# Performance work log

Hardware: AMD Instinct MI355X
Metric: run time of the kernel (lower is better)

The kernel has to match this reference:

```python
import jax, jax.numpy as jnp
import numpy as np

INPUT_DIM = 1024
NUM_HEADS = 16
HEAD_DIM = INPUT_DIM // NUM_HEADS


def setup_inputs() -> dict:
    key = jax.random.key(0)
    ks = jax.random.split(key, 9)
    d = INPUT_DIM
    s = 1.0 / np.sqrt(d)
    x = jax.random.normal(ks[0], (2, 2048, d), dtype=jnp.float32)
    # nn.Linear default init ~ U(-1/sqrt(in), 1/sqrt(in)); weights stored as (out, in), we keep (in, out)
    Wq = jax.random.uniform(ks[1], (d, d), jnp.float32, -s, s)
    bq = jax.random.uniform(ks[2], (d,), jnp.float32, -s, s)
    Wk = jax.random.uniform(ks[3], (d, d), jnp.float32, -s, s)
    bk = jax.random.uniform(ks[4], (d,), jnp.float32, -s, s)
    Wv = jax.random.uniform(ks[5], (d, d), jnp.float32, -s, s)
    bv = jax.random.uniform(ks[6], (d,), jnp.float32, -s, s)
    Wo = jax.random.uniform(ks[7], (d, d), jnp.float32, -s, s)
    bo = jax.random.uniform(ks[8], (d,), jnp.float32, -s, s)
    return {"x": x, "Wq": Wq, "bq": bq, "Wk": Wk, "bk": bk, "Wv": Wv, "bv": bv, "Wo": Wo, "bo": bo}


def reference(x, Wq, bq, Wk, bk, Wv, bv, Wo, bo):
    b, t, d = x.shape
    h, hd = NUM_HEADS, HEAD_DIM
    # projections -> [b, h, t, hd]
    q = (x @ Wq + bq).reshape(b, t, h, hd).transpose(0, 2, 1, 3)
    k = (x @ Wk + bk).reshape(b, t, h, hd).transpose(0, 2, 1, 3)
    v = (x @ Wv + bv).reshape(b, t, h, hd).transpose(0, 2, 1, 3)
    scores = jnp.einsum('bhqd,bhkd->bhqk', q, k) / jnp.sqrt(jnp.float32(hd))
    probs = jax.nn.softmax(scores, axis=-1)
    out = jnp.einsum('bhqk,bhkd->bhqd', probs, v)
    out = out.transpose(0, 2, 1, 3).reshape(b, t, d)
    return out @ Wo + bo
```

## Files before the change

kernel.cpp:

```cpp
#include <hip/hip_runtime.h>
#include <math.h>


#define BATCH 2
#define SEQ   2048
#define DIM   1024
#define NHEAD 16
#define HDIM  64
#define MROWS (BATCH * SEQ)
#define BH    (BATCH * NHEAD)
#define NSPLIT 2
#define TILES_PER_SPLIT (SEQ / 64 / NSPLIT)

typedef __attribute__((ext_vector_type(4))) float     floatx4;
typedef __attribute__((ext_vector_type(4))) float     float4v;
typedef __attribute__((ext_vector_type(8))) _Float16  half8;
typedef __attribute__((ext_vector_type(4))) _Float16  half4;
typedef __attribute__((ext_vector_type(2))) __fp16    fp16x2;
typedef __attribute__((ext_vector_type(4))) unsigned  uint4v;

#define SOFT_C 5.77078016f
#define QSCALE 0.18033688f

#if __has_builtin(__builtin_amdgcn_exp2f)
#define EXP2F(x) __builtin_amdgcn_exp2f(x)
#else
#define EXP2F(x) exp2f(x)
#endif

__device__ __forceinline__ void gload16(const void* g, void* l) {
    __builtin_amdgcn_global_load_lds(
        (const __attribute__((address_space(1))) unsigned int*)g,
        (__attribute__((address_space(3))) unsigned int*)l, 16, 0, 0);
}

__device__ __forceinline__ unsigned pk2(float a, float b) {
    fp16x2 v = __builtin_amdgcn_cvt_pkrtz(a, b);
    return __builtin_bit_cast(unsigned, v);
}

__device__ __forceinline__ void plswap(unsigned &a, unsigned &b) {
#if __has_builtin(__builtin_amdgcn_permlane32_swap) && __has_builtin(__builtin_amdgcn_permlane16_swap)
    auto r32 = __builtin_amdgcn_permlane32_swap(a, b, false, false);
    auto r16 = __builtin_amdgcn_permlane16_swap(r32[0], r32[1], false, false);
    a = r16[0]; b = r16[1];
#else
    asm volatile("s_nop 1\n\t"
                 "v_permlane32_swap_b32 %0, %1\n\t"
                 "s_nop 1\n\t"
                 "v_permlane16_swap_b32 %0, %1\n\t"
                 "s_nop 1"
                 : "+v"(a), "+v"(b));
#endif
}

__global__ __launch_bounds__(256) void prep(
    const float* __restrict__ x,
    const float* __restrict__ Wq, const float* __restrict__ Wk,
    const float* __restrict__ Wv, const float* __restrict__ Wo,
    _Float16* __restrict__ xh,
    _Float16* __restrict__ Wqt, _Float16* __restrict__ Wkt,
    _Float16* __restrict__ Wvt, _Float16* __restrict__ Wot)
{
    const int tid = threadIdx.x;
    if (blockIdx.z == 4) {
        const int bid = blockIdx.y * 16 + blockIdx.x;
        #pragma unroll
        for (int it = 0; it < 8; ++it) {
            const size_t i = (((size_t)it * 256 + bid) * 256 + tid) * 8;
            float4v a = *(const float4v*)(x + i);
            float4v b = *(const float4v*)(x + i + 4);
            half8 o;
            #pragma unroll
            for (int c = 0; c < 4; ++c) { o[c] = (_Float16)a[c]; o[4+c] = (_Float16)b[c]; }
            *(half8*)(xh + i) = o;
        }
        return;
    }
    __shared__ float tile[64][65];
    const float* W; _Float16* o;
    switch (blockIdx.z) {
        case 0: W = Wq; o = Wqt; break;
        case 1: W = Wk; o = Wkt; break;
        case 2: W = Wv; o = Wvt; break;
        default: W = Wo; o = Wot; break;
    }
    const int n0 = blockIdx.x * 64, k0 = blockIdx.y * 64;
    #pragma unroll
    for (int p = 0; p < 16; ++p) {
        int idx = tid + p * 256;
        int r = idx >> 6, c = idx & 63;
        tile[r][c] = W[(size_t)(k0 + r) * DIM + n0 + c];
    }
    __syncthreads();
    #pragma unroll
    for (int p = 0; p < 16; ++p) {
        int idx = tid + p * 256;
        int r = idx >> 6, c = idx & 63;
        o[(size_t)(n0 + r) * DIM + k0 + c] = (_Float16)tile[c][r];
    }
}

__device__ __forceinline__ void gemm_core16(
    const _Float16* __restrict__ Ap, const _Float16* __restrict__ Bp,
    int m0, int n0, _Float16* AL, _Float16* BL, floatx4 acc[4][4])
{
    const int tid  = threadIdx.x;
    const int wave = tid >> 6;
    const int lane = tid & 63;
    const int li   = lane & 15;
    const int quad = lane >> 4;
    const int wm   = (wave >> 1) * 64;
    const int wn   = (wave & 1) * 64;

    for (int kt = 0; kt < DIM / 64; ++kt) {
        __syncthreads();
        const int k0 = kt * 64;
        #pragma unroll
        for (int p = 0; p < 4; ++p) {
            int s = tid + p * 256;
            int r = s >> 3, ks = s & 7;
            int kg = (ks ^ (r & 7)) << 3;
            int ldsb = (wave * 64 + p * 256) * 8;
            gload16(Ap + (size_t)(m0 + r) * DIM + k0 + kg, AL + ldsb);
            gload16(Bp + (size_t)(n0 + r) * DIM + k0 + kg, BL + ldsb);
        }
        __syncthreads();

        half8 a[4][2], b[4][2];
        #pragma unroll
        for (int i = 0; i < 4; ++i) {
            int ra = (wm + i * 16 + li) << 6;
            int rb = (wn + i * 16 + li) << 6;
            #pragma unroll
            for (int h = 0; h < 2; ++h) {
                a[i][h] = *(const half8*)(AL + ra + (((h * 4 + quad) ^ (li & 7)) << 3));
                b[i][h] = *(const half8*)(BL + rb + (((h * 4 + quad) ^ (li & 7)) << 3));
            }
        }
        #pragma unroll
        for (int i = 0; i < 4; ++i)
            #pragma unroll
            for (int j = 0; j < 4; ++j) {
                acc[i][j] = __builtin_amdgcn_mfma_f32_16x16x32_f16(a[i][0], b[j][0], acc[i][j], 0, 0, 0);
                acc[i][j] = __builtin_amdgcn_mfma_f32_16x16x32_f16(a[i][1], b[j][1], acc[i][j], 0, 0, 0);
            }
    }
}

__global__ __launch_bounds__(256, 3) void qkv_mfma(
    const _Float16* __restrict__ xh,
    const _Float16* __restrict__ Wqt, const _Float16* __restrict__ Wkt,
    const _Float16* __restrict__ Wvt,
    const float* __restrict__ bq, const float* __restrict__ bk,
    const float* __restrict__ bv,
    _Float16* __restrict__ Qh, _Float16* __restrict__ Kh,
    _Float16* __restrict__ Vth)
{
    __shared__ __align__(16) _Float16 SH[128 * 128];
    _Float16* AL = SH;
    _Float16* BL = SH + 128 * 64;

    const int bid = blockIdx.x + 8 * (blockIdx.y + 32 * blockIdx.z);
    const int swz = (bid & 7) * 96 + (bid >> 3);
    const int bx  = swz & 7;
    const int by  = (swz >> 3) & 31;
    const int z   = swz >> 8;

    const _Float16* Bp; const float* bias;
    if (z == 0)      { Bp = Wqt; bias = bq; }
    else if (z == 1) { Bp = Wkt; bias = bk; }
    else             { Bp = Wvt; bias = bv; }

    const int m0 = by * 128, n0 = bx * 128;

    floatx4 acc[4][4];
    #pragma unroll
    for (int i = 0; i < 4; ++i)
        #pragma unroll
        for (int j = 0; j < 4; ++j) acc[i][j] = (floatx4){0.f, 0.f, 0.f, 0.f};

    gemm_core16(xh, Bp, m0, n0, AL, BL, acc);

    const int tid = threadIdx.x, wave = tid >> 6, lane = tid & 63;
    const int li = lane & 15, quad = lane >> 4;
    const int wm = (wave >> 1) * 64, wn = (wave & 1) * 64;
    const int bb = m0 >> 11, t0 = m0 & 2047;

    if (z != 2) {
        _Float16* out = (z == 0) ? Qh : Kh;
        const float sc = (z == 0) ? QSCALE : 1.0f;
        #pragma unroll
        for (int i = 0; i < 4; ++i)
            #pragma unroll
            for (int j = 0; j < 4; ++j) {
                int n = n0 + wn + j * 16 + li;
                int h = n >> 6, hd = n & 63;
                float b_ = bias[n];
                #pragma unroll
                for (int r = 0; r < 4; ++r) {
                    int m = m0 + wm + i * 16 + quad * 4 + r;
                    int t = m & 2047;
                    out[(((size_t)(bb * NHEAD + h) * SEQ) + t) * HDIM + hd] =
                        (_Float16)((acc[i][j][r] + b_) * sc);
                }
            }
    } else {
        __syncthreads();
        #pragma unroll
        for (int i = 0; i < 4; ++i)
            #pragma unroll
            for (int j = 0; j < 4; ++j) {
                int n = wn + j * 16 + li;
                float b_ = bias[n0 + n];
                half4 w;
                #pragma unroll
                for (int r = 0; r < 4; ++r) w[r] = (_Float16)(acc[i][j][r] + b_);
                int col  = wm + i * 16 + quad * 4;
                int colp = ((((col >> 3) ^ (n & 7)) << 3)) | (col & 7);
                *(half4*)(SH + n * 128 + colp) = w;
            }
        __syncthreads();
        #pragma unroll
        for (int p = 0; p < 8; ++p) {
            int idx = p * 256 + tid;
            int v = idx >> 4, c8 = (idx & 15) * 8;
            int c8p = (((c8 >> 3) ^ (v & 7)) << 3);
            half8 w = *(const half8*)(SH + v * 128 + c8p);
            int n = n0 + v;
            int h = n >> 6, hd = n & 63;
            *(half8*)(Vth + ((size_t)(bb * NHEAD + h) * HDIM + hd) * SEQ + t0 + c8) = w;
        }
    }
}

__global__ __launch_bounds__(256, 4) void attn(
    const _Float16* __restrict__ Q, const _Float16* __restrict__ K,
    const _Float16* __restrict__ Vt,
    _Float16* __restrict__ Op0, _Float16* __restrict__ Op1,
    float* __restrict__ rsb)
{
    __shared__ __align__(16) _Float16 Ks[2][64 * 64];
    __shared__ __align__(16) _Float16 Vs[2][64 * 64];

    const int tid  = threadIdx.x;
    const int wave = tid >> 6;
    const int lane = tid & 63;
    const int li   = lane & 15;
    const int quad = lane >> 4;

    const int bid = blockIdx.x + 16 * (blockIdx.y + 32 * blockIdx.z);
    const int swz = (bid & 7) * 128 + (bid >> 3);
    const int q0  = (swz & 15) * 128;
    const int bh  = (swz >> 4) & 31;
    const int z   = swz >> 9;
    const int b   = bh >> 4, h = bh & 15;

    half8 qa[2][2];
    #pragma unroll
    for (int nq = 0; nq < 2; ++nq) {
        size_t qrow = ((size_t)bh * SEQ + q0 + wave * 32 + nq * 16 + li) * HDIM;
        qa[nq][0] = *(const half8*)(Q + qrow + quad * 8);
        qa[nq][1] = *(const half8*)(Q + qrow + 32 + quad * 8);
    }

    half8 onesA;
    {
        _Float16 v = (li == 0) ? (_Float16)1.0f : (_Float16)0.0f;
        #pragma unroll
        for (int c = 0; c < 8; ++c) onesA[c] = v;
    }

    floatx4 O[4][2];
    floatx4 rsacc[2];
    #pragma unroll
    for (int nq = 0; nq < 2; ++nq) {
        rsacc[nq] = (floatx4){0.f, 0.f, 0.f, 0.f};
        #pragma unroll
        for (int i = 0; i < 4; ++i) O[i][nq] = (floatx4){0.f, 0.f, 0.f, 0.f};
    }

    const _Float16* Kbh = K  + (size_t)bh * SEQ * HDIM;
    const _Float16* Vbh = Vt + (size_t)bh * HDIM * SEQ;

    const int kt0 = z * TILES_PER_SPLIT, kt1 = kt0 + TILES_PER_SPLIT;

    auto stage = [&](int buf, int kt_) {
        const _Float16* Kg = Kbh + (size_t)kt_ * 64 * HDIM;
        const _Float16* Vg = Vbh + kt_ * 64;
        _Float16* Kl = &Ks[buf][0];
        _Float16* Vl = &Vs[buf][0];
        #pragma unroll
        for (int p = 0; p < 2; ++p) {
            int s = tid + p * 256;
            int r = s >> 3, ks = s & 7;
            int kg = (ks ^ (r & 7)) << 3;
            int ldsb = (wave * 64 + p * 256) * 8;
            gload16(Kg + r * HDIM + kg, Kl + ldsb);
            gload16(Vg + (size_t)r * SEQ + kg, Vl + ldsb);
        }
    };

    stage(0, kt0);
    __syncthreads();
    int cur = 0;

    for (int kt = kt0; kt < kt1; ++kt) {
        if (kt + 1 < kt1) stage(cur ^ 1, kt + 1);
        const _Float16* Kc = &Ks[cur][0];
        const _Float16* Vc = &Vs[cur][0];

        __builtin_amdgcn_s_setprio(1);

        unsigned R[2][4][2];
        #pragma unroll
        for (int mb = 0; mb < 4; ++mb) {
            int row = (mb * 16 + li) << 6;
            half8 a0 = *(const half8*)(Kc + row + ((quad ^ (li & 7)) << 3));
            half8 a1 = *(const half8*)(Kc + row + (((quad + 4) ^ (li & 7)) << 3));
            #pragma unroll
            for (int nq = 0; nq < 2; ++nq) {
                floatx4 st = (floatx4){-SOFT_C, -SOFT_C, -SOFT_C, -SOFT_C};
                st = __builtin_amdgcn_mfma_f32_16x16x32_f16(a0, qa[nq][0], st, 0, 0, 0);
                st = __builtin_amdgcn_mfma_f32_16x16x32_f16(a1, qa[nq][1], st, 0, 0, 0);
                R[nq][mb][0] = pk2(EXP2F(st[0]), EXP2F(st[1]));
                R[nq][mb][1] = pk2(EXP2F(st[2]), EXP2F(st[3]));
            }
        }

        half8 pb[2][2];
        #pragma unroll
        for (int nq = 0; nq < 2; ++nq)
            #pragma unroll
            for (int f = 0; f < 2; ++f) {
                unsigned w0, w1, w2, w3;
                {
                    unsigned x = R[nq][2 * f][0], y = R[nq][2 * f + 1][0];
                    plswap(x, y);
                    w0 = x; w2 = y;
                }
                {
                    unsigned x = R[nq][2 * f][1], y = R[nq][2 * f + 1][1];
                    plswap(x, y);
                    w1 = x; w3 = y;
                }
                uint4v uw; uw[0] = w0; uw[1] = w1; uw[2] = w2; uw[3] = w3;
                pb[nq][f] = __builtin_bit_cast(half8, uw);
            }

        #pragma unroll
        for (int nq = 0; nq < 2; ++nq) {
            rsacc[nq] = __builtin_amdgcn_mfma_f32_16x16x32_f16(onesA, pb[nq][0], rsacc[nq], 0, 0, 0);
            rsacc[nq] = __builtin_amdgcn_mfma_f32_16x16x32_f16(onesA, pb[nq][1], rsacc[nq], 0, 0, 0);
        }
        #pragma unroll
        for (int mb = 0; mb < 4; ++mb) {
            int row = (mb * 16 + li) << 6;
            half8 v0 = *(const half8*)(Vc + row + ((quad ^ (li & 7)) << 3));
            half8 v1 = *(const half8*)(Vc + row + (((quad + 4) ^ (li & 7)) << 3));
            #pragma unroll
            for (int nq = 0; nq < 2; ++nq) {
                O[mb][nq] = __builtin_amdgcn_mfma_f32_16x16x32_f16(v0, pb[nq][0], O[mb][nq], 0, 0, 0);
                O[mb][nq] = __builtin_amdgcn_mfma_f32_16x16x32_f16(v1, pb[nq][1], O[mb][nq], 0, 0, 0);
            }
        }

        __builtin_amdgcn_s_setprio(0);

        __syncthreads();
        cur ^= 1;
    }

    if (quad == 0) {
        #pragma unroll
        for (int nq = 0; nq < 2; ++nq)
            rsb[((size_t)z * BH + bh) * SEQ + q0 + wave * 32 + nq * 16 + li] = rsacc[nq][0];
    }

    _Float16* Op = (z == 0) ? Op0 : Op1;

    _Float16* Sw = &Ks[0][0] + wave * (32 * 64);
    #pragma unroll
    for (int mb = 0; mb < 4; ++mb)
        #pragma unroll
        for (int nq = 0; nq < 2; ++nq) {
            uint2 w;
            w.x = pk2(O[mb][nq][0], O[mb][nq][1]);
            w.y = pk2(O[mb][nq][2], O[mb][nq][3]);
            int row = nq * 16 + li;
            int col = mb * 16 + quad * 4;
            int swc = (((col >> 3) ^ (row & 7)) << 3) | (col & 7);
            *(uint2*)(Sw + row * 64 + swc) = w;
        }
    #pragma unroll
    for (int p = 0; p < 4; ++p) {
        int idx = p * 64 + lane;
        int qq = idx >> 3, c = idx & 7;
        half8 v = *(const half8*)(Sw + qq * 64 + ((c ^ (qq & 7)) << 3));
        size_t row = (size_t)b * SEQ + q0 + wave * 32 + qq;
        *(half8*)(Op + row * DIM + h * HDIM + c * 8) = v;
    }
}

__global__ __launch_bounds__(256) void combine(
    const _Float16* __restrict__ Op0, const _Float16* __restrict__ Op1,
    const float* __restrict__ rsb, _Float16* __restrict__ Ctx)
{
    const size_t idx8 = (size_t)blockIdx.x * 256 + threadIdx.x;
    const int m = (int)(idx8 >> 7);
    const int c = (int)(idx8 & 127);
    const int h = c >> 3;
    const int b = m >> 11, t = m & 2047;
    const size_t rsi = (size_t)(b * NHEAD + h) * SEQ + t;
    const float r0 = rsb[rsi];
    const float r1 = rsb[(size_t)BH * SEQ + rsi];
    const float inv = 1.0f / (r0 + r1);
    const size_t off = idx8 * 8;
    half8 o0 = *(const half8*)(Op0 + off);
    half8 o1 = *(const half8*)(Op1 + off);
    half8 o;
    #pragma unroll
    for (int r = 0; r < 8; ++r)
        o[r] = (_Float16)(((float)o0[r] + (float)o1[r]) * inv);
    *(half8*)(Ctx + off) = o;
}

__global__ __launch_bounds__(256, 3) void out_mfma(
    const _Float16* __restrict__ Ctx, const _Float16* __restrict__ Wot,
    const float* __restrict__ bo, float* __restrict__ out)
{
    __shared__ __align__(16) _Float16 AL[128 * 64];
    __shared__ __align__(16) _Float16 BL[128 * 64];

    const int bid = blockIdx.x + 8 * blockIdx.y;
    const int swz = (bid & 7) * 32 + (bid >> 3);
    const int m0 = (swz >> 3) * 128, n0 = (swz & 7) * 128;

    floatx4 acc[4][4];
    #pragma unroll
    for (int i = 0; i < 4; ++i)
        #pragma unroll
        for (int j = 0; j < 4; ++j) acc[i][j] = (floatx4){0.f, 0.f, 0.f, 0.f};

    gemm_core16(Ctx, Wot, m0, n0, AL, BL, acc);

    const int tid = threadIdx.x, wave = tid >> 6, lane = tid & 63;
    const int li = lane & 15, quad = lane >> 4;
    const int wm = (wave >> 1) * 64, wn = (wave & 1) * 64;

    #pragma unroll
    for (int i = 0; i < 4; ++i)
        #pragma unroll
        for (int j = 0; j < 4; ++j) {
            int n = n0 + wn + j * 16 + li;
            float b_ = bo[n];
            #pragma unroll
            for (int r = 0; r < 4; ++r) {
                int m = m0 + wm + i * 16 + quad * 4 + r;
                out[(size_t)m * DIM + n] = acc[i][j][r] + b_;
            }
        }
}

extern "C" void kernel_launch(void* const* d_in, const int* in_sizes, int n_in,
                              void* d_out, int out_size, void* d_ws, size_t ws_size,
                              hipStream_t stream) {
    const float* x  = (const float*)d_in[0];
    const float* Wq = (const float*)d_in[1];
    const float* bq = (const float*)d_in[2];
    const float* Wk = (const float*)d_in[3];
    const float* bk = (const float*)d_in[4];
    const float* Wv = (const float*)d_in[5];
    const float* bv = (const float*)d_in[6];
    const float* Wo = (const float*)d_in[7];
    const float* bo = (const float*)d_in[8];
    float* out = (float*)d_out;

    const size_t PX = (size_t)MROWS * DIM;
    const size_t PW = (size_t)DIM * DIM;
    _Float16* xh  = (_Float16*)d_ws;
    _Float16* Wqt = xh + PX;
    _Float16* Wkt = Wqt + PW;
    _Float16* Wvt = Wkt + PW;
    _Float16* Wot = Wvt + PW;
    _Float16* Qh  = Wot + PW;
    _Float16* Kh  = Qh + PX;
    _Float16* Op1 = Kh + PX;
    _Float16* Vth = Op1 + PX;

    _Float16* Op0 = xh;
    float*    rsb = (float*)Wqt;
    _Float16* Ctx = xh;

    prep<<<dim3(16, 16, 5), 256, 0, stream>>>(
        x, Wq, Wk, Wv, Wo, xh, Wqt, Wkt, Wvt, Wot);

    qkv_mfma<<<dim3(DIM / 128, MROWS / 128, 3), 256, 0, stream>>>(
        xh, Wqt, Wkt, Wvt, bq, bk, bv, Qh, Kh, Vth);

    attn<<<dim3(SEQ / 128, BH, NSPLIT), 256, 0, stream>>>(
        Qh, Kh, Vth, Op0, Op1, rsb);

    combine<<<dim3(PX / 8 / 256), 256, 0, stream>>>(Op0, Op1, rsb, Ctx);

    out_mfma<<<dim3(DIM / 128, MROWS / 128), 256, 0, stream>>>(
        Ctx, Wot, bo, out);
}
```

Before: 185.6 us.

## Fuse split-KV combine into output projection A-tile load

Removes the separate combine kernel and merges the two attention partial outputs directly while loading the A tile of the output GEMM. Each k-tile maps to one head, so the row-sum reciprocal is computed per row while staging into LDS. This drops a kernel launch and a full write plus read of the context tensor. In exchange, the A operand now goes through register loads and conversion instead of async global-to-LDS copies, and the partial outputs are re-read by each of the eight N-column blocks. Launch bounds on qkv_mfma and out_mfma are lowered from 3 to 2 blocks per CU to allow more registers.

```diff
diff --git a/kernel.cpp b/kernel.cpp
--- a/kernel.cpp
+++ b/kernel.cpp
@@ -148,7 +148,7 @@
     }
 }
 
-__global__ __launch_bounds__(256, 3) void qkv_mfma(
+__global__ __launch_bounds__(256, 2) void qkv_mfma(
     const _Float16* __restrict__ xh,
     const _Float16* __restrict__ Wqt, const _Float16* __restrict__ Wkt,
     const _Float16* __restrict__ Wvt,
@@ -402,31 +402,9 @@
     }
 }
 
-__global__ __launch_bounds__(256) void combine(
+__global__ __launch_bounds__(256, 2) void out_mfma(
     const _Float16* __restrict__ Op0, const _Float16* __restrict__ Op1,
-    const float* __restrict__ rsb, _Float16* __restrict__ Ctx)
-{
-    const size_t idx8 = (size_t)blockIdx.x * 256 + threadIdx.x;
-    const int m = (int)(idx8 >> 7);
-    const int c = (int)(idx8 & 127);
-    const int h = c >> 3;
-    const int b = m >> 11, t = m & 2047;
-    const size_t rsi = (size_t)(b * NHEAD + h) * SEQ + t;
-    const float r0 = rsb[rsi];
-    const float r1 = rsb[(size_t)BH * SEQ + rsi];
-    const float inv = 1.0f / (r0 + r1);
-    const size_t off = idx8 * 8;
-    half8 o0 = *(const half8*)(Op0 + off);
-    half8 o1 = *(const half8*)(Op1 + off);
-    half8 o;
-    #pragma unroll
-    for (int r = 0; r < 8; ++r)
-        o[r] = (_Float16)(((float)o0[r] + (float)o1[r]) * inv);
-    *(half8*)(Ctx + off) = o;
-}
-
-__global__ __launch_bounds__(256, 3) void out_mfma(
-    const _Float16* __restrict__ Ctx, const _Float16* __restrict__ Wot,
+    const float* __restrict__ rsb, const _Float16* __restrict__ Wot,
     const float* __restrict__ bo, float* __restrict__ out)
 {
     __shared__ __align__(16) _Float16 AL[128 * 64];
@@ -436,17 +414,70 @@
     const int swz = (bid & 7) * 32 + (bid >> 3);
     const int m0 = (swz >> 3) * 128, n0 = (swz & 7) * 128;
 
+    const int tid  = threadIdx.x;
+    const int wave = tid >> 6;
+    const int lane = tid & 63;
+    const int li   = lane & 15;
+    const int quad = lane >> 4;
+    const int wm   = (wave >> 1) * 64;
+    const int wn   = (wave & 1) * 64;
+
     floatx4 acc[4][4];
     #pragma unroll
     for (int i = 0; i < 4; ++i)
         #pragma unroll
         for (int j = 0; j < 4; ++j) acc[i][j] = (floatx4){0.f, 0.f, 0.f, 0.f};
 
-    gemm_core16(Ctx, Wot, m0, n0, AL, BL, acc);
-
-    const int tid = threadIdx.x, wave = tid >> 6, lane = tid & 63;
-    const int li = lane & 15, quad = lane >> 4;
-    const int wm = (wave >> 1) * 64, wn = (wave & 1) * 64;
+    for (int kt = 0; kt < DIM / 64; ++kt) {
+        __syncthreads();
+        const int k0 = kt * 64;
+        #pragma unroll
+        for (int p = 0; p < 4; ++p) {
+            int s = tid + p * 256;
+            int r = s >> 3, ks = s & 7;
+            int kg = (ks ^ (r & 7)) << 3;
+            int ldsb = (wave * 64 + p * 256) * 8;
+            gload16(Wot + (size_t)(n0 + r) * DIM + k0 + kg, BL + ldsb);
+        }
+        #pragma unroll
+        for (int p = 0; p < 4; ++p) {
+            int s = tid + p * 256;
+            int r = s >> 3, ks = s & 7;
+            int kg = (ks ^ (r & 7)) << 3;
+            int m = m0 + r;
+            int bb = m >> 11, t = m & 2047;
+            size_t rsi = (size_t)(bb * NHEAD + kt) * SEQ + t;
+            float inv = 1.0f / (rsb[rsi] + rsb[(size_t)BH * SEQ + rsi]);
+            size_t off = (size_t)m * DIM + k0 + kg;
+            half8 o0 = *(const half8*)(Op0 + off);
+            half8 o1 = *(const half8*)(Op1 + off);
+            half8 o;
+            #pragma unroll
+            for (int c = 0; c < 8; ++c)
+                o[c] = (_Float16)(((float)o0[c] + (float)o1[c]) * inv);
+            *(half8*)(AL + s * 8) = o;
+        }
+        __syncthreads();
+
+        half8 a[4][2], b[4][2];
+        #pragma unroll
+        for (int i = 0; i < 4; ++i) {
+            int ra = (wm + i * 16 + li) << 6;
+            int rb = (wn + i * 16 + li) << 6;
+            #pragma unroll
+            for (int h = 0; h < 2; ++h) {
+                a[i][h] = *(const half8*)(AL + ra + (((h * 4 + quad) ^ (li & 7)) << 3));
+                b[i][h] = *(const half8*)(BL + rb + (((h * 4 + quad) ^ (li & 7)) << 3));
+            }
+        }
+        #pragma unroll
+        for (int i = 0; i < 4; ++i)
+            #pragma unroll
+            for (int j = 0; j < 4; ++j) {
+                acc[i][j] = __builtin_amdgcn_mfma_f32_16x16x32_f16(a[i][0], b[j][0], acc[i][j], 0, 0, 0);
+                acc[i][j] = __builtin_amdgcn_mfma_f32_16x16x32_f16(a[i][1], b[j][1], acc[i][j], 0, 0, 0);
+            }
+    }
 
     #pragma unroll
     for (int i = 0; i < 4; ++i)
@@ -490,7 +521,6 @@
 
     _Float16* Op0 = xh;
     float*    rsb = (float*)Wqt;
-    _Float16* Ctx = xh;
 
     prep<<<dim3(16, 16, 5), 256, 0, stream>>>(
         x, Wq, Wk, Wv, Wo, xh, Wqt, Wkt, Wvt, Wot);
@@ -501,8 +531,6 @@
     attn<<<dim3(SEQ / 128, BH, NSPLIT), 256, 0, stream>>>(
         Qh, Kh, Vth, Op0, Op1, rsb);
 
-    combine<<<dim3(PX / 8 / 256), 256, 0, stream>>>(Op0, Op1, rsb, Ctx);
-
     out_mfma<<<dim3(DIM / 128, MROWS / 128), 256, 0, stream>>>(
-        Ctx, Wot, bo, out);
-}
+        Op0, Op1, rsb, Wot, bo, out);
+}
```

Result: slower. 195.2 us (+5.2%).

## Drop split-K attention and combine kernel; normalize output inside attn

Applied to the files above, without the earlier changes.

Removes the two-way key split in the attention kernel so each block processes all key tiles and normalizes its output by the row sum directly, which eliminates the separate combine kernel and the round trip of partial outputs and row sums through global memory. This halves the attention grid to 512 blocks on a 256-CU device, so parallelism per block grows longer and occupancy may drop. It also lowers the launch_bounds occupancy hint for the QKV and output GEMMs from 3 to 2, allowing more registers per thread at the cost of fewer resident waves.

```diff
diff --git a/kernel.cpp b/kernel.cpp
--- a/kernel.cpp
+++ b/kernel.cpp
@@ -9,8 +9,7 @@
 #define HDIM  64
 #define MROWS (BATCH * SEQ)
 #define BH    (BATCH * NHEAD)
-#define NSPLIT 2
-#define TILES_PER_SPLIT (SEQ / 64 / NSPLIT)
+#define NKT   (SEQ / 64)
 
 typedef __attribute__((ext_vector_type(4))) float     floatx4;
 typedef __attribute__((ext_vector_type(4))) float     float4v;
@@ -148,7 +147,7 @@
     }
 }
 
-__global__ __launch_bounds__(256, 3) void qkv_mfma(
+__global__ __launch_bounds__(256, 2) void qkv_mfma(
     const _Float16* __restrict__ xh,
     const _Float16* __restrict__ Wqt, const _Float16* __restrict__ Wkt,
     const _Float16* __restrict__ Wvt,
@@ -237,8 +236,7 @@
 __global__ __launch_bounds__(256, 4) void attn(
     const _Float16* __restrict__ Q, const _Float16* __restrict__ K,
     const _Float16* __restrict__ Vt,
-    _Float16* __restrict__ Op0, _Float16* __restrict__ Op1,
-    float* __restrict__ rsb)
+    _Float16* __restrict__ Ctx)
 {
     __shared__ __align__(16) _Float16 Ks[2][64 * 64];
     __shared__ __align__(16) _Float16 Vs[2][64 * 64];
@@ -249,11 +247,10 @@
     const int li   = lane & 15;
     const int quad = lane >> 4;
 
-    const int bid = blockIdx.x + 16 * (blockIdx.y + 32 * blockIdx.z);
-    const int swz = (bid & 7) * 128 + (bid >> 3);
+    const int bid = blockIdx.x + 16 * blockIdx.y;
+    const int swz = (bid & 7) * 64 + (bid >> 3);
     const int q0  = (swz & 15) * 128;
-    const int bh  = (swz >> 4) & 31;
-    const int z   = swz >> 9;
+    const int bh  = swz >> 4;
     const int b   = bh >> 4, h = bh & 15;
 
     half8 qa[2][2];
@@ -282,8 +279,6 @@
 
     const _Float16* Kbh = K  + (size_t)bh * SEQ * HDIM;
     const _Float16* Vbh = Vt + (size_t)bh * HDIM * SEQ;
-
-    const int kt0 = z * TILES_PER_SPLIT, kt1 = kt0 + TILES_PER_SPLIT;
 
     auto stage = [&](int buf, int kt_) {
         const _Float16* Kg = Kbh + (size_t)kt_ * 64 * HDIM;
@@ -301,12 +296,12 @@
         }
     };
 
-    stage(0, kt0);
+    stage(0, 0);
     __syncthreads();
     int cur = 0;
 
-    for (int kt = kt0; kt < kt1; ++kt) {
-        if (kt + 1 < kt1) stage(cur ^ 1, kt + 1);
+    for (int kt = 0; kt < NKT; ++kt) {
+        if (kt + 1 < NKT) stage(cur ^ 1, kt + 1);
         const _Float16* Kc = &Ks[cur][0];
         const _Float16* Vc = &Vs[cur][0];
 
@@ -371,13 +366,12 @@
         cur ^= 1;
     }
 
-    if (quad == 0) {
-        #pragma unroll
-        for (int nq = 0; nq < 2; ++nq)
-            rsb[((size_t)z * BH + bh) * SEQ + q0 + wave * 32 + nq * 16 + li] = rsacc[nq][0];
-    }
-
-    _Float16* Op = (z == 0) ? Op0 : Op1;
+    float inv[2];
+    #pragma unroll
+    for (int nq = 0; nq < 2; ++nq) {
+        float rs = __shfl(rsacc[nq][0], li, 64);
+        inv[nq] = 1.0f / rs;
+    }
 
     _Float16* Sw = &Ks[0][0] + wave * (32 * 64);
     #pragma unroll
@@ -385,47 +379,25 @@
         #pragma unroll
         for (int nq = 0; nq < 2; ++nq) {
             uint2 w;
-            w.x = pk2(O[mb][nq][0], O[mb][nq][1]);
-            w.y = pk2(O[mb][nq][2], O[mb][nq][3]);
+            w.x = pk2(O[mb][nq][0] * inv[nq], O[mb][nq][1] * inv[nq]);
+            w.y = pk2(O[mb][nq][2] * inv[nq], O[mb][nq][3] * inv[nq]);
             int row = nq * 16 + li;
             int col = mb * 16 + quad * 4;
             int swc = (((col >> 3) ^ (row & 7)) << 3) | (col & 7);
             *(uint2*)(Sw + row * 64 + swc) = w;
         }
+    __builtin_amdgcn_s_waitcnt(0);
     #pragma unroll
     for (int p = 0; p < 4; ++p) {
         int idx = p * 64 + lane;
         int qq = idx >> 3, c = idx & 7;
         half8 v = *(const half8*)(Sw + qq * 64 + ((c ^ (qq & 7)) << 3));
         size_t row = (size_t)b * SEQ + q0 + wave * 32 + qq;
-        *(half8*)(Op + row * DIM + h * HDIM + c * 8) = v;
-    }
-}
-
-__global__ __launch_bounds__(256) void combine(
-    const _Float16* __restrict__ Op0, const _Float16* __restrict__ Op1,
-    const float* __restrict__ rsb, _Float16* __restrict__ Ctx)
-{
-    const size_t idx8 = (size_t)blockIdx.x * 256 + threadIdx.x;
-    const int m = (int)(idx8 >> 7);
-    const int c = (int)(idx8 & 127);
-    const int h = c >> 3;
-    const int b = m >> 11, t = m & 2047;
-    const size_t rsi = (size_t)(b * NHEAD + h) * SEQ + t;
-    const float r0 = rsb[rsi];
-    const float r1 = rsb[(size_t)BH * SEQ + rsi];
-    const float inv = 1.0f / (r0 + r1);
-    const size_t off = idx8 * 8;
-    half8 o0 = *(const half8*)(Op0 + off);
-    half8 o1 = *(const half8*)(Op1 + off);
-    half8 o;
-    #pragma unroll
-    for (int r = 0; r < 8; ++r)
-        o[r] = (_Float16)(((float)o0[r] + (float)o1[r]) * inv);
-    *(half8*)(Ctx + off) = o;
-}
-
-__global__ __launch_bounds__(256, 3) void out_mfma(
+        *(half8*)(Ctx + row * DIM + h * HDIM + c * 8) = v;
+    }
+}
+
+__global__ __launch_bounds__(256, 2) void out_mfma(
     const _Float16* __restrict__ Ctx, const _Float16* __restrict__ Wot,
     const float* __restrict__ bo, float* __restrict__ out)
 {
@@ -485,11 +457,9 @@
     _Float16* Wot = Wvt + PW;
     _Float16* Qh  = Wot + PW;
     _Float16* Kh  = Qh + PX;
-    _Float16* Op1 = Kh + PX;
-    _Float16* Vth = Op1 + PX;
-
-    _Float16* Op0 = xh;
-    float*    rsb = (float*)Wqt;
+    _Float16* spare = Kh + PX;
+    _Float16* Vth = spare + PX;
+
     _Float16* Ctx = xh;
 
     prep<<<dim3(16, 16, 5), 256, 0, stream>>>(
@@ -498,10 +468,8 @@
     qkv_mfma<<<dim3(DIM / 128, MROWS / 128, 3), 256, 0, stream>>>(
         xh, Wqt, Wkt, Wvt, bq, bk, bv, Qh, Kh, Vth);
 
-    attn<<<dim3(SEQ / 128, BH, NSPLIT), 256, 0, stream>>>(
-        Qh, Kh, Vth, Op0, Op1, rsb);
-
-    combine<<<dim3(PX / 8 / 256), 256, 0, stream>>>(Op0, Op1, rsb, Ctx);
+    attn<<<dim3(SEQ / 128, BH), 256, 0, stream>>>(
+        Qh, Kh, Vth, Ctx);
 
     out_mfma<<<dim3(DIM / 128, MROWS / 128), 256, 0, stream>>>(
         Ctx, Wot, bo, out);
```

New measurement: 179.7 us. 3.2% less time.
